# Kernel tuning notes

Hardware: AMD Instinct MI355X
Metric: run time of the kernel (lower is better)

## Reference

```python
import jax, jax.numpy as jnp
import numpy as np

V, NLAB, NLAYERS, DI, DM, DS, DD, K = 32000, 9, 2, 768, 1536, 16, 96, 4
B, S = 2, 2048
EPS = 1e-6


def setup_inputs() -> dict:
    key = jax.random.key(0)
    ks = jax.random.split(key, 12)
    n = lambda k, shape, s=0.02: jax.random.normal(k, shape, jnp.float32) * s
    return {
        "input_ids": jax.random.randint(ks[0], (B, S), 0, V, dtype=jnp.int32),
        "attention_mask": jnp.ones((B, S), jnp.int32),
        "emb": n(ks[1], (V, DI)),
        "norm_w": jnp.ones((NLAYERS, DI), jnp.float32),
        "in_proj_w": n(ks[2], (NLAYERS, 2 * DM, DI)),
        "conv_w": n(ks[3], (NLAYERS, DM, K), 0.1),
        "conv_b": jnp.zeros((NLAYERS, DM), jnp.float32),
        "sB_w": n(ks[4], (NLAYERS, DS, DM)),
        "sC_w": n(ks[5], (NLAYERS, DS, DM)),
        "sD1_w": n(ks[6], (NLAYERS, DD, DM)),
        "sD2_w": n(ks[7], (NLAYERS, DM, DD)),
        "A": jnp.tile(jnp.arange(1, DS + 1, dtype=jnp.float32), (NLAYERS, DM, 1)),
        "Dp": jnp.ones((NLAYERS, DM), jnp.float32),
        "out_w": n(ks[8], (NLAYERS, DI, DM)),
        "cls_w": n(ks[9], (NLAB, DI)),
        "cls_b": jnp.zeros((NLAB,), jnp.float32),
    }


def _rmsnorm(x, w):
    return x * jax.lax.rsqrt(jnp.mean(x * x, axis=-1, keepdims=True) + EPS) * w


def _mamba_block(x, norm_w, Wi, cw, cb, WB, WC, W1, W2, A, Dp, Wo):
    # x: (b, l, d_input)
    h = _rmsnorm(x, norm_w)
    a, gate = jnp.split(h @ Wi.T, 2, axis=-1)  # each (b, l, DM)
    # causal depthwise conv1d, kernel K, left-pad K-1 (== Conv1d(pad=K-1)[..., :l])
    L = a.shape[1]
    ap = jnp.pad(a, ((0, 0), (K - 1, 0), (0, 0)))
    conv = cb + sum(ap[:, i:i + L, :] * cw[:, i] for i in range(K))
    a = jax.nn.silu(conv)
    # selective SSM
    Bm = a @ WB.T                                   # (b, l, DS)
    Cm = a @ WC.T                                   # (b, l, DS)
    delta = jax.nn.softplus(Dp + (a @ W1.T) @ W2.T)  # (b, l, DM)
    A_bar = jnp.exp(delta[..., None] * (-A))         # (b, l, DM, DS)
    X_bar = (delta * a)[..., None] * Bm[:, :, None, :]  # (b, l, DM, DS)

    def comb(c1, c2):
        a1, x1 = c1
        a2, x2 = c2
        return a1 * a2, a2 * x1 + x2

    _, hid = jax.lax.associative_scan(comb, (A_bar, X_bar), axis=1)
    y = jnp.einsum('blds,bls->bld', hid, Cm) + Dp * a
    y = y * jax.nn.silu(gate)
    return y @ Wo.T


def _forward(input_ids, attention_mask, emb, norm_w, in_proj_w, conv_w, conv_b,
             sB_w, sC_w, sD1_w, sD2_w, A, Dp, out_w, cls_w, cls_b):
    x = emb[input_ids] * attention_mask[..., None].astype(emb.dtype)
    for i in range(NLAYERS):  # residual Mamba layers
        x = _mamba_block(x, norm_w[i], in_proj_w[i], conv_w[i], conv_b[i],
                         sB_w[i], sC_w[i], sD1_w[i], sD2_w[i], A[i], Dp[i], out_w[i]) + x
    # dropout is identity at inference
    return x @ cls_w.T + cls_b  # logits (b, l, num_labels)


def reference(input_ids, attention_mask, emb, norm_w, in_proj_w, conv_w, conv_b,
              sB_w, sC_w, sD1_w, sD2_w, A, Dp, out_w, cls_w, cls_b):
    return _forward(input_ids, attention_mask, emb, norm_w, in_proj_w, conv_w, conv_b,
                    sB_w, sC_w, sD1_w, sD2_w, A, Dp, out_w, cls_w, cls_b)
```

## Files before the change

kernel.cpp:

```cpp
#include <hip/hip_runtime.h>
#include <hip/hip_bf16.h>
#include <math.h>

#define NLAB 9
#define NL   2
#define DI   768
#define DM   1536
#define DS   16
#define KC   4
#define DD   96
#define BB   2
#define SS   2048
#define TT   (BB*SS)
#define EPSF 1e-6f

#define NCH  64
#define CL   (SS/NCH)

#define NW   128
#define KS   8
#define KSL  (DM/KS)

typedef __attribute__((ext_vector_type(4))) float f32x4;
typedef __attribute__((ext_vector_type(8))) short bf16x8;
typedef __attribute__((ext_vector_type(4))) unsigned short us4;

__device__ __forceinline__ float siluf(float x) { return x / (1.f + __expf(-x)); }
__device__ __forceinline__ float softplusf(float x) { return x > 15.f ? x : log1pf(__expf(x)); }

__device__ __forceinline__ unsigned short f2bf(float f) {
    unsigned u = __float_as_uint(f);
    return (unsigned short)((u + 0x7fffu + ((u >> 16) & 1u)) >> 16);
}
__device__ __forceinline__ float bf2f(unsigned short s) {
    return __uint_as_float((unsigned)s << 16);
}

__device__ __forceinline__ void xcd_map(int gx, int gy, int bx, int by,
                                        int& bmt, int& bnt)
{
    int flat = by * gx + bx;
    if ((gx & 1) == 0 && (gy & 3) == 0) {
        int halfx = gx >> 1, quarty = gy >> 2;
        int xcd = flat & 7, local = flat >> 3;
        bnt = (xcd & 1) * halfx + local % halfx;
        bmt = (xcd >> 1) * quarty + local / halfx;
    } else { bmt = by; bnt = bx; }
}

__global__ void f32_to_bf16(const float* __restrict__ src,
                            unsigned short* __restrict__ dst, int n)
{
    int i = (blockIdx.x * 256 + threadIdx.x) * 8;
    if (i >= n) return;
    float4 a = *(const float4*)(src + i);
    float4 b = *(const float4*)(src + i + 4);
    union { unsigned short s[8]; uint4 v; } o;
    o.s[0] = f2bf(a.x); o.s[1] = f2bf(a.y); o.s[2] = f2bf(a.z); o.s[3] = f2bf(a.w);
    o.s[4] = f2bf(b.x); o.s[5] = f2bf(b.y); o.s[6] = f2bf(b.z); o.s[7] = f2bf(b.w);
    *(uint4*)(dst + i) = o.v;
}

__global__ void embed_kernel(const int* __restrict__ ids, const int* __restrict__ mask,
                             const float* __restrict__ emb, float* __restrict__ x)
{
    int t = blockIdx.x;
    int i = threadIdx.x;
    float m = (float)mask[t];
    int id = ids[t];
    float4 v = ((const float4*)(emb + (size_t)id * DI))[i];
    v.x *= m; v.y *= m; v.z *= m; v.w *= m;
    ((float4*)(x + (size_t)t * DI))[i] = v;
}

__global__ void rmsnorm_kernel(const float* __restrict__ x, const float* __restrict__ w,
                               unsigned short* __restrict__ h)
{
    __shared__ float red[4];
    int t = blockIdx.x;
    const float* xr = x + (size_t)t * DI;
    float ss = 0.f;
    for (int i = threadIdx.x; i < DI; i += 256) { float v = xr[i]; ss += v * v; }
    #pragma unroll
    for (int m = 1; m < 64; m <<= 1) ss += __shfl_xor(ss, m, 64);
    if ((threadIdx.x & 63) == 0) red[threadIdx.x >> 6] = ss;
    __syncthreads();
    float scale = rsqrtf((red[0] + red[1] + red[2] + red[3]) * (1.f / DI) + EPSF);
    for (int i = threadIdx.x; i < DI; i += 256)
        h[(size_t)t * DI + i] = f2bf(xr[i] * scale * w[i]);
}

#define STAGE_TILE(AS, BS, KT) do {                                                           \
    _Pragma("unroll")                                                                         \
    for (int it = 0; it < 2; ++it) {                                                          \
        int rbase = it * 64 + wave * 16;                                                      \
        int row = rbase + (lane >> 2);                                                        \
        int c8 = (((lane & 3) ^ ((lane >> 3) & 3)) * 8);                                      \
        __builtin_amdgcn_global_load_lds(                                                     \
            (const __attribute__((address_space(1))) unsigned int*)(Arow + (size_t)row * lda + (KT) + c8), \
            (__attribute__((address_space(3))) unsigned int*)((AS) + rbase * 32), 16, 0, 0);  \
        __builtin_amdgcn_global_load_lds(                                                     \
            (const __attribute__((address_space(1))) unsigned int*)(Brow + (size_t)row * ldb + (KT) + c8), \
            (__attribute__((address_space(3))) unsigned int*)((BS) + rbase * 32), 16, 0, 0);  \
    } } while (0)

#define COMPUTE_TILE(AS, BS) do {                                                             \
    bf16x8 af[4], bfr[4];                                                                     \
    const int khs = (kh ^ ((lr >> 1) & 3)) * 8;                                               \
    _Pragma("unroll")                                                                         \
    for (int i = 0; i < 4; ++i)                                                               \
        af[i] = *(const bf16x8*)&(AS)[(wm + i * 16 + lr) * 32 + khs];                         \
    _Pragma("unroll")                                                                         \
    for (int j = 0; j < 4; ++j)                                                               \
        bfr[j] = *(const bf16x8*)&(BS)[(wn + j * 16 + lr) * 32 + khs];                        \
    _Pragma("unroll")                                                                         \
    for (int i = 0; i < 4; ++i)                                                               \
        _Pragma("unroll")                                                                     \
        for (int j = 0; j < 4; ++j)                                                           \
            acc[i][j] = __builtin_amdgcn_mfma_f32_16x16x32_bf16(af[i], bfr[j], acc[i][j], 0, 0, 0); \
    } while (0)

#define WAIT_BAR(T, NT) do {                                                                  \
    if ((T) + 1 < (NT)) asm volatile("s_waitcnt vmcnt(4)" ::: "memory");                      \
    else                asm volatile("s_waitcnt vmcnt(0)" ::: "memory");                      \
    __builtin_amdgcn_s_barrier();                                                             \
} while (0)

__global__ __launch_bounds__(256) void gemm_bf16(
    const unsigned short* __restrict__ A, const unsigned short* __restrict__ B,
    const float* __restrict__ Rres, const float* __restrict__ bias,
    float* __restrict__ C, int M, int N, int K,
    int lda, int ldb, int ldc, int act, int out16)
{
    __shared__ unsigned short As0[128 * 32];
    __shared__ unsigned short Bs0[128 * 32];
    __shared__ unsigned short As1[128 * 32];
    __shared__ unsigned short Bs1[128 * 32];
    __shared__ unsigned short As2[128 * 32];
    __shared__ unsigned short Bs2[128 * 32];
    const int tid = threadIdx.x;
    const int wave = tid >> 6, lane = tid & 63;

    int bmt, bnt;
    xcd_map(gridDim.x, gridDim.y, blockIdx.x, blockIdx.y, bmt, bnt);
    const int bm = bmt * 128, bn = bnt * 128;

    const int wm = (wave >> 1) * 64, wn = (wave & 1) * 64;
    const int lr = lane & 15, kh = lane >> 4;

    f32x4 acc[4][4] = {};

    const unsigned short* Arow = A + (size_t)bm * lda;
    const unsigned short* Brow = B + (size_t)bn * ldb;

    const int nt = K >> 5;
    STAGE_TILE(As0, Bs0, 0);
    if (nt > 1) STAGE_TILE(As1, Bs1, 32);

    int t = 0;
    while (true) {
        WAIT_BAR(t, nt);
        if (t + 2 < nt) STAGE_TILE(As2, Bs2, (t + 2) * 32);
        COMPUTE_TILE(As0, Bs0);
        if (++t == nt) break;
        WAIT_BAR(t, nt);
        if (t + 2 < nt) STAGE_TILE(As0, Bs0, (t + 2) * 32);
        COMPUTE_TILE(As1, Bs1);
        if (++t == nt) break;
        WAIT_BAR(t, nt);
        if (t + 2 < nt) STAGE_TILE(As1, Bs1, (t + 2) * 32);
        COMPUTE_TILE(As2, Bs2);
        if (++t == nt) break;
    }

    #pragma unroll
    for (int i = 0; i < 4; ++i) {
        #pragma unroll
        for (int j = 0; j < 4; ++j) {
            #pragma unroll
            for (int r = 0; r < 4; ++r) {
                int row = bm + wm + i * 16 + kh * 4 + r;
                int col = bn + wn + j * 16 + lr;
                float v = acc[i][j][r];
                if (bias) v += bias[col];
                if (act == 1) v = softplusf(v);
                if (Rres) v += Rres[(size_t)row * ldc + col];
                if (out16)
                    ((unsigned short*)C)[(size_t)row * ldc + col] = f2bf(v);
                else
                    C[(size_t)row * ldc + col] = v;
            }
        }
    }
}

__global__ __launch_bounds__(256) void gemm_skinny_bf16(
    const unsigned short* __restrict__ A, const unsigned short* __restrict__ B,
    float* __restrict__ Part)
{
    __shared__ unsigned short As0[128 * 32];
    __shared__ unsigned short Bs0[128 * 32];
    __shared__ unsigned short As1[128 * 32];
    __shared__ unsigned short Bs1[128 * 32];
    __shared__ unsigned short As2[128 * 32];
    __shared__ unsigned short Bs2[128 * 32];
    const int tid = threadIdx.x;
    const int wave = tid >> 6, lane = tid & 63;
    const int bm = blockIdx.x * 128;
    const int ks = blockIdx.y;
    const int k0 = ks * KSL;
    const int wm = (wave >> 1) * 64, wn = (wave & 1) * 64;
    const int lr = lane & 15, kh = lane >> 4;
    const int lda = DM, ldb = DM;

    f32x4 acc[4][4] = {};

    const unsigned short* Arow = A + (size_t)bm * DM;
    const unsigned short* Brow = B;

    const int nt = KSL >> 5;
    STAGE_TILE(As0, Bs0, k0);
    STAGE_TILE(As1, Bs1, k0 + 32);

    int t = 0;
    while (true) {
        WAIT_BAR(t, nt);
        if (t + 2 < nt) STAGE_TILE(As2, Bs2, k0 + (t + 2) * 32);
        COMPUTE_TILE(As0, Bs0);
        if (++t == nt) break;
        WAIT_BAR(t, nt);
        if (t + 2 < nt) STAGE_TILE(As0, Bs0, k0 + (t + 2) * 32);
        COMPUTE_TILE(As1, Bs1);
        if (++t == nt) break;
        WAIT_BAR(t, nt);
        if (t + 2 < nt) STAGE_TILE(As1, Bs1, k0 + (t + 2) * 32);
        COMPUTE_TILE(As2, Bs2);
        if (++t == nt) break;
    }

    float* out = Part + (size_t)ks * TT * NW;
    #pragma unroll
    for (int i = 0; i < 4; ++i) {
        #pragma unroll
        for (int j = 0; j < 4; ++j) {
            #pragma unroll
            for (int r = 0; r < 4; ++r) {
                int row = bm + wm + i * 16 + kh * 4 + r;
                int col = wn + j * 16 + lr;
                out[(size_t)row * NW + col] = acc[i][j][r];
            }
        }
    }
}

__global__ void skinny_reduce(const float* __restrict__ Part,
                              float* __restrict__ BCD, unsigned short* __restrict__ dd16)
{
    int idx = blockIdx.x * 256 + threadIdx.x;
    float s = 0.f;
    #pragma unroll
    for (int ks = 0; ks < KS; ++ks)
        s += Part[(size_t)ks * TT * NW + idx];
    BCD[idx] = s;
    int col = idx & (NW - 1);
    if (col >= 32)
        dd16[(size_t)(idx >> 7) * DD + (col - 32)] = f2bf(s);
}

__global__ __launch_bounds__(192) void conv_silu_kernel(
    const unsigned short* __restrict__ proj16, const float* __restrict__ cw,
    const float* __restrict__ cb, unsigned short* __restrict__ aconv16)
{
    int t = blockIdx.x;
    int d0 = threadIdx.x * 8;
    int p = t & (SS - 1);

    float4 w[8];
    #pragma unroll
    for (int k = 0; k < 8; ++k) w[k] = ((const float4*)cw)[d0 + k];
    float acc[8];
    #pragma unroll
    for (int k = 0; k < 8; ++k) acc[k] = cb[d0 + k];

    #pragma unroll
    for (int j = 0; j < KC; ++j) {
        int pp = p - (KC - 1) + j;
        if (pp >= 0) {
            const unsigned short* rowp = proj16 + (size_t)(t - (KC - 1) + j) * (2 * DM) + d0;
            us4 lo = *(const us4*)rowp;
            us4 hi = *(const us4*)(rowp + 4);
            #pragma unroll
            for (int k = 0; k < 4; ++k) {
                acc[k]     += (&w[k].x)[j]     * bf2f(lo[k]);
                acc[4 + k] += (&w[4 + k].x)[j] * bf2f(hi[k]);
            }
        }
    }
    union { unsigned short s[8]; uint4 v; } o;
    #pragma unroll
    for (int k = 0; k < 8; ++k) o.s[k] = f2bf(siluf(acc[k]));
    *(uint4*)(aconv16 + (size_t)t * DM + d0) = o.v;
}

__global__ void concat_w_kernel(const float* __restrict__ WB, const float* __restrict__ WC,
                                const float* __restrict__ W1, unsigned short* __restrict__ Wcat16)
{
    int l = blockIdx.y;
    int row = blockIdx.x;
    const float* src;
    if (row < 16)      src = WB + (size_t)l * DS * DM + (size_t)row * DM;
    else if (row < 32) src = WC + (size_t)l * DS * DM + (size_t)(row - 16) * DM;
    else               src = W1 + (size_t)l * DD * DM + (size_t)(row - 32) * DM;
    unsigned short* dst = Wcat16 + ((size_t)l * NW + row) * DM;
    for (int i = threadIdx.x; i < DM / 4; i += 256) {
        float4 v = ((const float4*)src)[i];
        us4 u = { f2bf(v.x), f2bf(v.y), f2bf(v.z), f2bf(v.w) };
        *(us4*)(dst + i * 4) = u;
    }
}

__global__ __launch_bounds__(256) void scan_pass1(
    const float* __restrict__ dtv, const unsigned short* __restrict__ av16,
    const float* __restrict__ BCD, const float* __restrict__ Amat,
    float2* __restrict__ PQ)
{
    __shared__ float4 sB4[CL][DS / 4];
    int b = blockIdx.z, c = blockIdx.y;
    int d = blockIdx.x * 256 + threadIdx.x;
    size_t rowbase = (size_t)b * SS + (size_t)c * CL;

    for (int i = threadIdx.x; i < CL * DS; i += 256)
        ((float*)sB4)[i] = BCD[(rowbase + (i >> 4)) * NW + (i & 15)];
    __syncthreads();

    float negA[DS], hid[DS];
    #pragma unroll
    for (int s = 0; s < DS; ++s) {
        negA[s] = -Amat[(size_t)d * DS + s];
        hid[s] = 0.f;
    }
    float cum = 0.f;

    const float* pd = dtv + rowbase * DM + d;
    const unsigned short* pa = av16 + rowbase * DM + d;
    for (int t = 0; t < CL; ++t) {
        float dt = pd[(size_t)t * DM];
        float avv = bf2f(pa[(size_t)t * DM]);
        cum += dt;
        float xv = dt * avv;
        #pragma unroll
        for (int j = 0; j < DS / 4; ++j) {
            float4 bv = sB4[t][j];
            hid[4*j+0] = __expf(dt * negA[4*j+0]) * hid[4*j+0] + xv * bv.x;
            hid[4*j+1] = __expf(dt * negA[4*j+1]) * hid[4*j+1] + xv * bv.y;
            hid[4*j+2] = __expf(dt * negA[4*j+2]) * hid[4*j+2] + xv * bv.z;
            hid[4*j+3] = __expf(dt * negA[4*j+3]) * hid[4*j+3] + xv * bv.w;
        }
    }
    float2* out = PQ + ((size_t)(b * NCH + c) * DM + d) * DS;
    #pragma unroll
    for (int s = 0; s < DS; ++s)
        out[s] = make_float2(__expf(cum * negA[s]), hid[s]);
}

__global__ void scan_carry(float2* __restrict__ PQ)
{
    int idx = blockIdx.x * 256 + threadIdx.x;
    int b = idx / (DM * DS);
    int r = idx - b * (DM * DS);
    float2* base = PQ + (size_t)b * NCH * (DM * DS) + r;
    float carry = 0.f;
    for (int cb = 0; cb < NCH; cb += 8) {
        float2 v[8];
        #pragma unroll
        for (int j = 0; j < 8; ++j)
            v[j] = base[(size_t)(cb + j) * (DM * DS)];
        #pragma unroll
        for (int j = 0; j < 8; ++j) {
            base[(size_t)(cb + j) * (DM * DS)].x = carry;
            carry = v[j].x * carry + v[j].y;
        }
    }
}

__global__ __launch_bounds__(256) void scan_pass2(
    const float* __restrict__ dtv, const unsigned short* __restrict__ av16,
    const float* __restrict__ BCD,
    const unsigned short* __restrict__ proj16, const float* __restrict__ Amat,
    const float* __restrict__ Dp, const float2* __restrict__ PQ,
    unsigned short* __restrict__ y)
{
    __shared__ float4 sB4[CL][DS / 4];
    __shared__ float4 sC4[CL][DS / 4];
    int b = blockIdx.z, c = blockIdx.y;
    int d = blockIdx.x * 256 + threadIdx.x;
    size_t rowbase = (size_t)b * SS + (size_t)c * CL;

    for (int i = threadIdx.x; i < CL * DS; i += 256) {
        size_t row = rowbase + (i >> 4);
        ((float*)sB4)[i] = BCD[row * NW + (i & 15)];
        ((float*)sC4)[i] = BCD[row * NW + 16 + (i & 15)];
    }
    __syncthreads();

    float negA[DS], hid[DS];
    const float2* pin = PQ + ((size_t)(b * NCH + c) * DM + d) * DS;
    #pragma unroll
    for (int s = 0; s < DS; ++s) {
        negA[s] = -Amat[(size_t)d * DS + s];
        hid[s] = pin[s].x;
    }
    float Dpd = Dp[d];

    const float* pd = dtv + rowbase * DM + d;
    const unsigned short* pa = av16 + rowbase * DM + d;
    const unsigned short* gp = proj16 + rowbase * (2 * DM) + DM + d;
    unsigned short* yp = y + rowbase * DM + d;

    for (int t = 0; t < CL; ++t) {
        float dt = pd[(size_t)t * DM];
        float avv = bf2f(pa[(size_t)t * DM]);
        float g  = bf2f(gp[(size_t)t * (2 * DM)]);
        float xv = dt * avv;
        float acc0 = 0.f, acc1 = 0.f, acc2 = 0.f, acc3 = 0.f;
        #pragma unroll
        for (int j = 0; j < DS / 4; ++j) {
            float4 bv = sB4[t][j];
            float4 cv = sC4[t][j];
            hid[4*j+0] = __expf(dt * negA[4*j+0]) * hid[4*j+0] + xv * bv.x;
            hid[4*j+1] = __expf(dt * negA[4*j+1]) * hid[4*j+1] + xv * bv.y;
            hid[4*j+2] = __expf(dt * negA[4*j+2]) * hid[4*j+2] + xv * bv.z;
            hid[4*j+3] = __expf(dt * negA[4*j+3]) * hid[4*j+3] + xv * bv.w;
            acc0 += hid[4*j+0] * cv.x;
            acc1 += hid[4*j+1] * cv.y;
            acc2 += hid[4*j+2] * cv.z;
            acc3 += hid[4*j+3] * cv.w;
        }
        float contrib = (acc0 + acc1) + (acc2 + acc3);
        yp[(size_t)t * DM] = f2bf((contrib + Dpd * avv) * siluf(g));
    }
}

__global__ void cls_kernel(const float* __restrict__ x, const float* __restrict__ W,
                           const float* __restrict__ bias, float* __restrict__ out)
{
    int t = blockIdx.x;
    int lane = threadIdx.x;
    const float* xr = x + (size_t)t * DI;
    float acc[NLAB];
    #pragma unroll
    for (int n = 0; n < NLAB; ++n) acc[n] = 0.f;
    for (int i = lane; i < DI; i += 64) {
        float xv = xr[i];
        #pragma unroll
        for (int n = 0; n < NLAB; ++n) acc[n] += xv * W[(size_t)n * DI + i];
    }
    #pragma unroll
    for (int n = 0; n < NLAB; ++n)
        #pragma unroll
        for (int m = 1; m < 64; m <<= 1) acc[n] += __shfl_xor(acc[n], m, 64);
    if (lane < NLAB) out[(size_t)t * NLAB + lane] = acc[lane] + bias[lane];
}

extern "C" void kernel_launch(void* const* d_in, const int* in_sizes, int n_in,
                              void* d_out, int out_size, void* d_ws, size_t ws_size,
                              hipStream_t stream)
{
    const int*   ids    = (const int*)d_in[0];
    const int*   mask   = (const int*)d_in[1];
    const float* emb    = (const float*)d_in[2];
    const float* norm_w = (const float*)d_in[3];
    const float* Wi     = (const float*)d_in[4];
    const float* conv_w = (const float*)d_in[5];
    const float* conv_b = (const float*)d_in[6];
    const float* sB_w   = (const float*)d_in[7];
    const float* sC_w   = (const float*)d_in[8];
    const float* sD1_w  = (const float*)d_in[9];
    const float* sD2_w  = (const float*)d_in[10];
    const float* Amat   = (const float*)d_in[11];
    const float* Dp     = (const float*)d_in[12];
    const float* out_w  = (const float*)d_in[13];
    const float* cls_w  = (const float*)d_in[14];
    const float* cls_b  = (const float*)d_in[15];
    float* logits = (float*)d_out;

    float* ws = (float*)d_ws;
    size_t off = 0;
    float* x     = ws + off; off += (size_t)TT * DI;
    unsigned short* proj16 = (unsigned short*)(ws + off); off += (size_t)TT * 2 * DM / 2;
    float* dtv   = ws + off; off += (size_t)TT * DM;
    float* BCD   = ws + off; off += (size_t)TT * NW;
    size_t scratch_sz = (size_t)BB * NCH * DM * DS * 2;
    size_t part_sz = (size_t)KS * TT * NW;
    if (part_sz > scratch_sz) scratch_sz = part_sz;
    float* Part  = ws + off;
    float2* PQ   = (float2*)(ws + off); off += scratch_sz;
    unsigned short* y16     = (unsigned short*)(ws + off); off += (size_t)TT * DM / 2;
    unsigned short* aconv16 = (unsigned short*)(ws + off); off += (size_t)TT * DM / 2;
    unsigned short* Wi16    = (unsigned short*)(ws + off); off += (size_t)NL * 2 * DM * DI / 2;
    unsigned short* Wo16    = (unsigned short*)(ws + off); off += (size_t)NL * DI * DM / 2;
    unsigned short* W216    = (unsigned short*)(ws + off); off += (size_t)NL * DM * DD / 2;
    unsigned short* dd16    = (unsigned short*)(ws + off); off += (size_t)TT * DD / 2;
    unsigned short* Wcat16  = (unsigned short*)(ws + off); off += (size_t)NL * NW * DM / 2;
    if (ws_size < off * sizeof(float)) return;

    unsigned short* h16 = (unsigned short*)dtv;

    embed_kernel<<<TT, DI / 4, 0, stream>>>(ids, mask, emb, x);
    concat_w_kernel<<<dim3(NW, NL), 256, 0, stream>>>(sB_w, sC_w, sD1_w, Wcat16);

    f32_to_bf16<<<(NL * 2 * DM * DI / 8 + 255) / 256, 256, 0, stream>>>(Wi, Wi16, NL * 2 * DM * DI);
    f32_to_bf16<<<(NL * DI * DM / 8 + 255) / 256, 256, 0, stream>>>(out_w, Wo16, NL * DI * DM);
    f32_to_bf16<<<(NL * DM * DD / 8 + 255) / 256, 256, 0, stream>>>(sD2_w, W216, NL * DM * DD);

    for (int l = 0; l < NL; ++l) {
        const float* cw_l  = conv_w + (size_t)l * DM * KC;
        const float* cb_l  = conv_b + (size_t)l * DM;
        const float* A_l   = Amat  + (size_t)l * DM * DS;
        const float* Dp_l  = Dp    + (size_t)l * DM;
        const float* nw_l  = norm_w + (size_t)l * DI;
        const unsigned short* Wi16_l  = Wi16  + (size_t)l * 2 * DM * DI;
        const unsigned short* Wo16_l  = Wo16  + (size_t)l * DI * DM;
        const unsigned short* W216_l  = W216  + (size_t)l * DM * DD;
        const unsigned short* Wcat16_l = Wcat16 + (size_t)l * NW * DM;

        rmsnorm_kernel<<<TT, 256, 0, stream>>>(x, nw_l, h16);

        gemm_bf16<<<dim3(2 * DM / 128, TT / 128), 256, 0, stream>>>(
            h16, Wi16_l, nullptr, nullptr, (float*)proj16, TT, 2 * DM, DI, DI, DI, 2 * DM, 0, 1);

        conv_silu_kernel<<<TT, DM / 8, 0, stream>>>(proj16, cw_l, cb_l, aconv16);

        gemm_skinny_bf16<<<dim3(TT / 128, KS), 256, 0, stream>>>(aconv16, Wcat16_l, Part);
        skinny_reduce<<<TT * NW / 256, 256, 0, stream>>>(Part, BCD, dd16);

        gemm_bf16<<<dim3(DM / 128, TT / 128), 256, 0, stream>>>(
            dd16, W216_l, nullptr, Dp_l, dtv, TT, DM, DD, DD, DD, DM, 1, 0);

        scan_pass1<<<dim3(DM / 256, NCH, BB), 256, 0, stream>>>(dtv, aconv16, BCD, A_l, PQ);
        scan_carry<<<BB * DM * DS / 256, 256, 0, stream>>>(PQ);
        scan_pass2<<<dim3(DM / 256, NCH, BB), 256, 0, stream>>>(
            dtv, aconv16, BCD, proj16, A_l, Dp_l, PQ, y16);

        gemm_bf16<<<dim3(DI / 128, TT / 128), 256, 0, stream>>>(
            y16, Wo16_l, x, nullptr, x, TT, DI, DM, DM, DM, DI, 0, 0);
    }

    cls_kernel<<<TT, 64, 0, stream>>>(x, cls_w, cls_b, logits);
}
```

Baseline: 801.0 us.

## Fuse split-K reduction with delta projection and softplus into one kernel

The split-K reduction kernel now also computes the delta projection, replacing the separate MFMA GEMM launch and the bf16 dd intermediate buffer. Each block reduces four tokens' partial sums and stages the 96-wide dd vectors in shared memory. Each thread then computes six output channels with scalar FMAs against bf16 W2 rows and applies softplus, writing dtv directly. This removes a kernel launch and the dd round trip through global memory. In exchange, the delta GEMM moves off matrix cores onto scalar FMA, and every block re-reads the whole W2 matrix with per-thread row loads that do not coalesce well.

```diff
diff --git a/kernel.cpp b/kernel.cpp
--- a/kernel.cpp
+++ b/kernel.cpp
@@ -253,18 +253,61 @@
     }
 }
 
-__global__ void skinny_reduce(const float* __restrict__ Part,
-                              float* __restrict__ BCD, unsigned short* __restrict__ dd16)
-{
-    int idx = blockIdx.x * 256 + threadIdx.x;
-    float s = 0.f;
-    #pragma unroll
-    for (int ks = 0; ks < KS; ++ks)
-        s += Part[(size_t)ks * TT * NW + idx];
-    BCD[idx] = s;
-    int col = idx & (NW - 1);
-    if (col >= 32)
-        dd16[(size_t)(idx >> 7) * DD + (col - 32)] = f2bf(s);
+__global__ __launch_bounds__(256) void skinny_reduce_delta(
+    const float* __restrict__ Part, const unsigned short* __restrict__ W2,
+    const float* __restrict__ Dp, float* __restrict__ BCD, float* __restrict__ dtv)
+{
+    __shared__ float sddT[DD][4];
+    const int t0 = blockIdx.x * 4;
+
+    #pragma unroll
+    for (int q = 0; q < 2; ++q) {
+        int idx = blockIdx.x * 512 + q * 256 + threadIdx.x;
+        float s = 0.f;
+        #pragma unroll
+        for (int ks = 0; ks < KS; ++ks)
+            s += Part[(size_t)ks * TT * NW + idx];
+        int col = idx & (NW - 1);
+        int rl  = (idx >> 7) & 3;
+        if (col < 32) BCD[idx] = s;
+        else          sddT[col - 32][rl] = s;
+    }
+    __syncthreads();
+
+    #pragma unroll
+    for (int kp = 0; kp < 3; ++kp) {
+        int da = (2 * kp) * 256 + threadIdx.x;
+        int db = da + 256;
+        const uint4* wa = (const uint4*)(W2 + (size_t)da * DD);
+        const uint4* wb = (const uint4*)(W2 + (size_t)db * DD);
+        uint4 va[12], vb[12];
+        #pragma unroll
+        for (int i = 0; i < 12; ++i) { va[i] = wa[i]; vb[i] = wb[i]; }
+        float dpa = Dp[da], dpb = Dp[db];
+        float acca[4], accb[4];
+        #pragma unroll
+        for (int r = 0; r < 4; ++r) { acca[r] = dpa; accb[r] = dpb; }
+        #pragma unroll
+        for (int i = 0; i < 12; ++i) {
+            const unsigned short* pa = (const unsigned short*)&va[i];
+            const unsigned short* pb = (const unsigned short*)&vb[i];
+            #pragma unroll
+            for (int e = 0; e < 8; ++e) {
+                int ii = i * 8 + e;
+                float4 sv = *(const float4*)&sddT[ii][0];
+                float wfa = bf2f(pa[e]), wfb = bf2f(pb[e]);
+                acca[0] += sv.x * wfa; acca[1] += sv.y * wfa;
+                acca[2] += sv.z * wfa; acca[3] += sv.w * wfa;
+                accb[0] += sv.x * wfb; accb[1] += sv.y * wfb;
+                accb[2] += sv.z * wfb; accb[3] += sv.w * wfb;
+            }
+        }
+        #pragma unroll
+        for (int r = 0; r < 4; ++r) {
+            dtv[(size_t)(t0 + r) * DM + da] = softplusf(acca[r]);
+            dtv[(size_t)(t0 + r) * DM + db] = softplusf(accb[r]);
+        }
+    }
 }
 
 __global__ __launch_bounds__(192) void conv_silu_kernel(
@@ -500,7 +543,6 @@
     unsigned short* Wi16    = (unsigned short*)(ws + off); off += (size_t)NL * 2 * DM * DI / 2;
     unsigned short* Wo16    = (unsigned short*)(ws + off); off += (size_t)NL * DI * DM / 2;
     unsigned short* W216    = (unsigned short*)(ws + off); off += (size_t)NL * DM * DD / 2;
-    unsigned short* dd16    = (unsigned short*)(ws + off); off += (size_t)TT * DD / 2;
     unsigned short* Wcat16  = (unsigned short*)(ws + off); off += (size_t)NL * NW * DM / 2;
     if (ws_size < off * sizeof(float)) return;
 
@@ -532,10 +574,7 @@
         conv_silu_kernel<<<TT, DM / 8, 0, stream>>>(proj16, cw_l, cb_l, aconv16);
 
         gemm_skinny_bf16<<<dim3(TT / 128, KS), 256, 0, stream>>>(aconv16, Wcat16_l, Part);
-        skinny_reduce<<<TT * NW / 256, 256, 0, stream>>>(Part, BCD, dd16);
-
-        gemm_bf16<<<dim3(DM / 128, TT / 128), 256, 0, stream>>>(
-            dd16, W216_l, nullptr, Dp_l, dtv, TT, DM, DD, DD, DD, DM, 1, 0);
+        skinny_reduce_delta<<<TT / 4, 256, 0, stream>>>(Part, W216_l, Dp_l, BCD, dtv);
 
         scan_pass1<<<dim3(DM / 256, NCH, BB), 256, 0, stream>>>(dtv, aconv16, BCD, A_l, PQ);
         scan_carry<<<BB * DM * DS / 256, 256, 0, stream>>>(PQ);
```

After: 1.209 ms. 50.9% more time.
